# Performance work log

Hardware: AMD Instinct MI355X
Metric: run time of the kernel (lower is better)

The kernel has to match this reference:

```python
import jax, jax.numpy as jnp
import numpy as np


def _sage_conv(x_src, x_dst, esrc, edst, num_dst, W_l, b_l, W_r):
    # PyG SAGEConv (aggr='mean'): out = lin_l(mean_{j->i} x_j) + lin_r(x_i)
    msg = x_src[esrc]                                   # [E, F] gather
    agg = jax.ops.segment_sum(msg, edst, num_segments=num_dst)
    cnt = jax.ops.segment_sum(jnp.ones((esrc.shape[0],), x_src.dtype), edst,
                              num_segments=num_dst)
    mean = agg / jnp.maximum(cnt, 1.0)[:, None]         # [num_dst, F]
    return mean @ W_l + b_l + x_dst @ W_r


def setup_inputs() -> dict:
    key = jax.random.key(0)
    ks = jax.random.split(key, 12)
    N_TOTAL, F_IN, HID, OUT = 1500000, 128, 256, 128
    NS0, ND0, NS1, ND1 = 1441792, 90112, 90112, 8192
    E0, E1 = 1351680, 81920
    x_all = jax.random.normal(ks[0], (N_TOTAL, F_IN), dtype=jnp.float32)
    n_id = jax.random.randint(ks[1], (NS0,), 0, N_TOTAL, dtype=jnp.int64)
    edge_src0 = jax.random.randint(ks[2], (E0,), 0, NS0, dtype=jnp.int64)
    edge_dst0 = jax.random.randint(ks[3], (E0,), 0, ND0, dtype=jnp.int64)
    edge_src1 = jax.random.randint(ks[4], (E1,), 0, NS1, dtype=jnp.int64)
    edge_dst1 = jax.random.randint(ks[5], (E1,), 0, ND1, dtype=jnp.int64)
    s0 = 1.0 / np.sqrt(F_IN)
    s1 = 1.0 / np.sqrt(HID)
    W_l0 = jax.random.normal(ks[6], (F_IN, HID), dtype=jnp.float32) * s0
    b_l0 = jnp.zeros((HID,), dtype=jnp.float32)
    W_r0 = jax.random.normal(ks[7], (F_IN, HID), dtype=jnp.float32) * s0
    W_l1 = jax.random.normal(ks[8], (HID, OUT), dtype=jnp.float32) * s1
    b_l1 = jnp.zeros((OUT,), dtype=jnp.float32)
    W_r1 = jax.random.normal(ks[9], (HID, OUT), dtype=jnp.float32) * s1
    return {
        "x_all": x_all, "n_id": n_id,
        "edge_src0": edge_src0, "edge_dst0": edge_dst0,
        "edge_src1": edge_src1, "edge_dst1": edge_dst1,
        "W_l0": W_l0, "b_l0": b_l0, "W_r0": W_r0,
        "W_l1": W_l1, "b_l1": b_l1, "W_r1": W_r1,
        "num_src0": NS0, "num_dst0": ND0, "num_src1": NS1, "num_dst1": ND1,
    }


def reference(x_all, n_id, edge_src0, edge_dst0, edge_src1, edge_dst1,
              W_l0, b_l0, W_r0, W_l1, b_l1, W_r1,
              num_src0, num_dst0, num_src1, num_dst1):
    x = x_all[n_id]                                     # [num_src0, F_in]
    # Layer 1 (block 0): bipartite SAGEConv + ReLU
    x = _sage_conv(x[:num_src0], x[:num_dst0], edge_src0, edge_dst0,
                   num_dst0, W_l0, b_l0, W_r0)
    x = jax.nn.relu(x)                                  # [num_dst0, hid]
    # Layer 2 (block 1): final SAGEConv, no activation
    x = _sage_conv(x[:num_src1], x[:num_dst1], edge_src1, edge_dst1,
                   num_dst1, W_l1, b_l1, W_r1)
    return x                                            # [num_dst1, out]
```

## Files before the change

kernel.cpp:

```cpp
#include <hip/hip_runtime.h>

#define ND0 90112
#define ND1 8192
#define NDT (ND0 + ND1)
#define NE0 1351680
#define NE1 81920
#define NET (NE0 + NE1)
#define F_IN 128
#define HID 256
#define F_OUT 128
#define BCAP 64

typedef __attribute__((ext_vector_type(8))) short short8;
typedef __attribute__((ext_vector_type(4))) float f32x4;

__device__ inline ushort f2bf(float f) {
    unsigned u = __float_as_uint(f);
    return (ushort)((u + 0x7fffu + ((u >> 16) & 1u)) >> 16);
}
__device__ inline float bf2f(ushort h) {
    return __uint_as_float(((unsigned)h) << 16);
}

__global__ void bucket_scatter_k(const int* __restrict__ esrc0, const int* __restrict__ edst0,
                                 const int* __restrict__ esrc1, const int* __restrict__ edst1,
                                 const int* __restrict__ nid, int* __restrict__ cnt,
                                 int* __restrict__ bkt) {
    int e = blockIdx.x * 256 + threadIdx.x;
    if (e >= NET) return;
    int d, s;
    if (e < NE0) {
        d = edst0[e];
        s = nid[esrc0[e]];
    } else {
        int e1 = e - NE0;
        d = ND0 + edst1[e1];
        s = esrc1[e1];
    }
    int pos = atomicAdd(&cnt[d], 1);
    if (pos < BCAP) bkt[(size_t)d * BCAP + pos] = s;
}

__global__ void wtrans_all_k(const float* __restrict__ Wl0, const float* __restrict__ Wr0,
                             const float* __restrict__ Wl1, const float* __restrict__ Wr1,
                             ushort* __restrict__ Bt0, ushort* __restrict__ Bt1) {
    int idx = blockIdx.x * 256 + threadIdx.x;
    constexpr int N0 = HID * 2 * F_IN;
    if (idx < N0) {
        int K2 = 2 * F_IN;
        int n = idx / K2, k = idx - n * K2;
        float v = (k < F_IN) ? Wl0[(size_t)k * HID + n] : Wr0[(size_t)(k - F_IN) * HID + n];
        Bt0[idx] = f2bf(v);
    } else {
        int j = idx - N0;
        int K2 = 2 * HID;
        int n = j / K2, k = j - n * K2;
        float v = (k < HID) ? Wl1[(size_t)k * F_OUT + n] : Wr1[(size_t)(k - HID) * F_OUT + n];
        Bt1[j] = f2bf(v);
    }
}

__global__ __launch_bounds__(512, 4) void fused1_k(
    const float* __restrict__ X, const int* __restrict__ bkt,
    const int* __restrict__ cnt, const int* __restrict__ nid,
    const ushort* __restrict__ Bt, const float* __restrict__ bias,
    ushort* __restrict__ C) {
    __shared__ ushort As[64][264];
    __shared__ ushort Bs[64][72];
    __shared__ int s_num[64];

    int t = threadIdx.x;
    int row0 = blockIdx.x * 64;

    if (t < 64) s_num[t] = cnt[row0 + t];
    __syncthreads();

    {
        int row = t >> 3, q = t & 7;
        int gr = nid[row0 + row];
        const float* gp = &X[(size_t)gr * F_IN + q * 16];
#pragma unroll
        for (int i = 0; i < 2; ++i) {
            float4 v0 = *(const float4*)(gp + i * 8);
            float4 v1 = *(const float4*)(gp + i * 8 + 4);
            short8 o;
            o[0] = (short)f2bf(v0.x); o[1] = (short)f2bf(v0.y);
            o[2] = (short)f2bf(v0.z); o[3] = (short)f2bf(v0.w);
            o[4] = (short)f2bf(v1.x); o[5] = (short)f2bf(v1.y);
            o[6] = (short)f2bf(v1.z); o[7] = (short)f2bf(v1.w);
            *(short8*)&As[row][F_IN + q * 16 + i * 8] = o;
        }
    }

    {
        int u = t & 3;
        int slot = (t >> 2) & 3;
        int rloc = t >> 4;
#pragma unroll 1
        for (int pass = 0; pass < 2; ++pass) {
            int row = pass * 32 + rloc;
            int beg = (row0 + row) * BCAP;
            int num = s_num[row];
            float acc[32] = {};
#pragma unroll 1
            for (int e = slot; e < num; e += 4) {
                int r = bkt[beg + e];
                const float* rp = &X[(size_t)r * F_IN + u * 4];
#pragma unroll
                for (int i = 0; i < 8; ++i) {
                    float4 v = *(const float4*)(rp + i * 16);
                    acc[i * 4 + 0] += v.x;
                    acc[i * 4 + 1] += v.y;
                    acc[i * 4 + 2] += v.z;
                    acc[i * 4 + 3] += v.w;
                }
            }
#pragma unroll
            for (int i = 0; i < 32; ++i) {
                acc[i] += __shfl_xor(acc[i], 4);
                acc[i] += __shfl_xor(acc[i], 8);
            }
            if (slot == 0) {
                float inv = 1.f / (float)((num > 0) ? num : 1);
#pragma unroll
                for (int i = 0; i < 8; ++i) {
                    ushort4 o;
                    o.x = f2bf(acc[i * 4 + 0] * inv);
                    o.y = f2bf(acc[i * 4 + 1] * inv);
                    o.z = f2bf(acc[i * 4 + 2] * inv);
                    o.w = f2bf(acc[i * 4 + 3] * inv);
                    *(ushort4*)&As[row][i * 16 + u * 4] = o;
                }
            }
        }
    }

    int lane = t & 63;
    int w = t >> 6;
    int wm = w >> 2, wn2 = w & 3;
    int lr = lane & 15, lj = lane >> 4;
    int bn = t >> 3, bk = (t & 7) * 8;

    for (int nt = 0; nt < 4; ++nt) {
        f32x4 acc2[2] = {};
        for (int k0 = 0; k0 < 256; k0 += 64) {
            short8 bv = *(const short8*)&Bt[(size_t)(nt * 64 + bn) * 256 + k0 + bk];
            __syncthreads();
            *(short8*)&Bs[bn][bk] = bv;
            __syncthreads();
#pragma unroll
            for (int ks = 0; ks < 64; ks += 32) {
                short8 bf = *(const short8*)&Bs[wn2 * 16 + lr][ks + lj * 8];
#pragma unroll
                for (int mi = 0; mi < 2; ++mi) {
                    short8 af = *(const short8*)&As[wm * 32 + mi * 16 + lr][k0 + ks + lj * 8];
                    acc2[mi] = __builtin_amdgcn_mfma_f32_16x16x32_bf16(af, bf, acc2[mi], 0, 0, 0);
                }
            }
        }
        int c = nt * 64 + wn2 * 16 + lr;
        float bi = bias[c];
#pragma unroll
        for (int mi = 0; mi < 2; ++mi) {
#pragma unroll
            for (int j = 0; j < 4; ++j) {
                int r = row0 + wm * 32 + mi * 16 + lj * 4 + j;
                float v = acc2[mi][j] + bi;
                v = fmaxf(v, 0.f);
                C[(size_t)r * HID + c] = f2bf(v);
            }
        }
    }
}

template <int F>
__global__ __launch_bounds__(128) void agg_k(
    const ushort* __restrict__ Xh, const int* __restrict__ bkt,
    const int* __restrict__ cnt, int dofs, ushort* __restrict__ mean) {
    __shared__ float sh[128][8];
    int d = blockIdx.x;
    int t = threadIdx.x;
    int cg = t & 31, slot = t >> 5;
    int beg = (dofs + d) * BCAP;
    int num = cnt[dofs + d];
    float acc[8] = {};
    for (int e = 0; e < num; e += 8) {
        int i0 = e + slot, i1 = e + 4 + slot;
        bool v0 = i0 < num, v1 = i1 < num;
        int r0 = v0 ? bkt[beg + i0] : 0;
        int r1 = v1 ? bkt[beg + i1] : 0;
        if (v0) {
            short8 x = *(const short8*)&Xh[(size_t)r0 * F + cg * 8];
#pragma unroll
            for (int i = 0; i < 8; ++i) acc[i] += bf2f((ushort)x[i]);
        }
        if (v1) {
            short8 x = *(const short8*)&Xh[(size_t)r1 * F + cg * 8];
#pragma unroll
            for (int i = 0; i < 8; ++i) acc[i] += bf2f((ushort)x[i]);
        }
    }
#pragma unroll
    for (int i = 0; i < 8; ++i) sh[t][i] = acc[i];
    __syncthreads();
    if (t < 32) {
        float inv = 1.f / (float)((num > 0) ? num : 1);
        short8 ov;
#pragma unroll
        for (int i = 0; i < 8; ++i) {
            float s = sh[t][i] + sh[t + 32][i] + sh[t + 64][i] + sh[t + 96][i];
            ov[i] = (short)f2bf(s * inv);
        }
        *(short8*)&mean[(size_t)d * F + t * 8] = ov;
    }
}

template <int BM, int KHALF, int NCOLS, bool RELU, bool OUT_BF16>
__global__ __launch_bounds__(256) void mgemm_k(
    const ushort* __restrict__ A0, const ushort* __restrict__ A1,
    const ushort* __restrict__ Bt, const float* __restrict__ bias,
    void* __restrict__ Cv, int M) {
    constexpr int MI = BM / 32;
    constexpr int TPR = 256 / BM;
    constexpr int AV = 64 / TPR / 8;
    __shared__ ushort As[BM][72];
    __shared__ ushort Bs[64][72];

    int t = threadIdx.x;
    int row0 = blockIdx.x * BM;
    int col0 = blockIdx.y * 64;
    int lane = t & 63;
    int w = t >> 6, wm = w >> 1, wn = w & 1;
    int lr = lane & 15;
    int lk = (lane >> 4) * 8;

    int ar = t / TPR, ac = (t % TPR) * (64 / TPR);
    int bn = t >> 2, bc = (t & 3) * 16;

    f32x4 acc[MI][2] = {};

    for (int k0 = 0; k0 < 2 * KHALF; k0 += 64) {
        const ushort* Asrc = (k0 < KHALF) ? A0 : A1;
        int kof = (k0 < KHALF) ? k0 : (k0 - KHALF);
        const ushort* ap = &Asrc[(size_t)(row0 + ar) * KHALF + kof + ac];
        const ushort* bp = &Bt[(size_t)(col0 + bn) * (2 * KHALF) + k0 + bc];
        short8 av[AV];
#pragma unroll
        for (int i = 0; i < AV; ++i) av[i] = *(const short8*)(ap + 8 * i);
        short8 bv0 = *(const short8*)(bp);
        short8 bv1 = *(const short8*)(bp + 8);
        __syncthreads();
#pragma unroll
        for (int i = 0; i < AV; ++i) *(short8*)&As[ar][ac + 8 * i] = av[i];
        *(short8*)&Bs[bn][bc + 0] = bv0;
        *(short8*)&Bs[bn][bc + 8] = bv1;
        __syncthreads();
#pragma unroll
        for (int ks = 0; ks < 64; ks += 32) {
            short8 bf0 = *(const short8*)&Bs[wn * 32 + lr][ks + lk];
            short8 bf1 = *(const short8*)&Bs[wn * 32 + 16 + lr][ks + lk];
#pragma unroll
            for (int mi = 0; mi < MI; ++mi) {
                short8 af = *(const short8*)&As[wm * (BM / 2) + mi * 16 + lr][ks + lk];
                acc[mi][0] = __builtin_amdgcn_mfma_f32_16x16x32_bf16(af, bf0, acc[mi][0], 0, 0, 0);
                acc[mi][1] = __builtin_amdgcn_mfma_f32_16x16x32_bf16(af, bf1, acc[mi][1], 0, 0, 0);
            }
        }
    }

    int orow = row0 + wm * (BM / 2);
    int ocol = col0 + wn * 32;
#pragma unroll
    for (int mi = 0; mi < MI; ++mi) {
#pragma unroll
        for (int ni = 0; ni < 2; ++ni) {
            int c = ocol + ni * 16 + lr;
            float bi = bias[c];
#pragma unroll
            for (int j = 0; j < 4; ++j) {
                int r = orow + mi * 16 + (lane >> 4) * 4 + j;
                float v = acc[mi][ni][j] + bi;
                if (RELU) v = fmaxf(v, 0.f);
                if (OUT_BF16)
                    ((ushort*)Cv)[(size_t)r * NCOLS + c] = f2bf(v);
                else
                    ((float*)Cv)[(size_t)r * NCOLS + c] = v;
            }
        }
    }
}

extern "C" void kernel_launch(void* const* d_in, const int* in_sizes, int n_in,
                              void* d_out, int out_size, void* d_ws, size_t ws_size,
                              hipStream_t stream) {
    const float* x_all = (const float*)d_in[0];
    const int* n_id = (const int*)d_in[1];
    const int* esrc0 = (const int*)d_in[2];
    const int* edst0 = (const int*)d_in[3];
    const int* esrc1 = (const int*)d_in[4];
    const int* edst1 = (const int*)d_in[5];
    const float* W_l0 = (const float*)d_in[6];
    const float* b_l0 = (const float*)d_in[7];
    const float* W_r0 = (const float*)d_in[8];
    const float* W_l1 = (const float*)d_in[9];
    const float* b_l1 = (const float*)d_in[10];
    const float* W_r1 = (const float*)d_in[11];

    char* ws = (char*)d_ws;
    size_t off = 0;
    auto alloc = [&](size_t bytes) {
        off = (off + 255) & ~(size_t)255;
        void* p = ws + off;
        off += bytes;
        return p;
    };
    int* cnt = (int*)alloc((size_t)NDT * 4);
    int* bkt = (int*)alloc((size_t)NDT * BCAP * 4);
    ushort* h = (ushort*)alloc((size_t)ND0 * HID * 2);
    ushort* mean1 = (ushort*)alloc((size_t)ND1 * HID * 2);
    ushort* Bt0 = (ushort*)alloc((size_t)HID * (2 * F_IN) * 2);
    ushort* Bt1 = (ushort*)alloc((size_t)F_OUT * (2 * HID) * 2);

    hipMemsetAsync(cnt, 0, (size_t)NDT * 4, stream);

    wtrans_all_k<<<512, 256, 0, stream>>>(W_l0, W_r0, W_l1, W_r1, Bt0, Bt1);
    bucket_scatter_k<<<(NET + 255) / 256, 256, 0, stream>>>(esrc0, edst0, esrc1,
                                                            edst1, n_id, cnt, bkt);

    fused1_k<<<ND0 / 64, 512, 0, stream>>>(x_all, bkt, cnt, n_id, Bt0, b_l0, h);

    agg_k<HID><<<ND1, 128, 0, stream>>>(h, bkt, cnt, ND0, mean1);
    mgemm_k<64, HID, F_OUT, false, false>
        <<<dim3(ND1 / 64, F_OUT / 64), 256, 0, stream>>>(mean1, h, Bt1, b_l1,
                                                         (float*)d_out, ND1);
}
```

Before: 239.6 us.

## Merge prep kernels, software-pipeline layer-1 gather, fuse layer-2 aggregate with GEMM

```diff
diff --git a/kernel.cpp b/kernel.cpp
--- a/kernel.cpp
+++ b/kernel.cpp
@@ -10,6 +10,7 @@
 #define HID 256
 #define F_OUT 128
 #define BCAP 64
+#define WT_BLOCKS 512
 
 typedef __attribute__((ext_vector_type(8))) short short8;
 typedef __attribute__((ext_vector_type(4))) float f32x4;
@@ -22,41 +23,44 @@
     return __uint_as_float(((unsigned)h) << 16);
 }
 
-__global__ void bucket_scatter_k(const int* __restrict__ esrc0, const int* __restrict__ edst0,
-                                 const int* __restrict__ esrc1, const int* __restrict__ edst1,
-                                 const int* __restrict__ nid, int* __restrict__ cnt,
-                                 int* __restrict__ bkt) {
-    int e = blockIdx.x * 256 + threadIdx.x;
-    if (e >= NET) return;
-    int d, s;
-    if (e < NE0) {
-        d = edst0[e];
-        s = nid[esrc0[e]];
+__global__ void prep_k(const float* __restrict__ Wl0, const float* __restrict__ Wr0,
+                       const float* __restrict__ Wl1, const float* __restrict__ Wr1,
+                       ushort* __restrict__ Bt0, ushort* __restrict__ Bt1,
+                       const int* __restrict__ esrc0, const int* __restrict__ edst0,
+                       const int* __restrict__ esrc1, const int* __restrict__ edst1,
+                       const int* __restrict__ nid, int* __restrict__ cnt,
+                       int* __restrict__ bkt) {
+    if (blockIdx.x < WT_BLOCKS) {
+        int idx = blockIdx.x * 256 + threadIdx.x;
+        constexpr int N0 = HID * 2 * F_IN;
+        if (idx < N0) {
+            int K2 = 2 * F_IN;
+            int n = idx / K2, k = idx - n * K2;
+            float v = (k < F_IN) ? Wl0[(size_t)k * HID + n]
+                                 : Wr0[(size_t)(k - F_IN) * HID + n];
+            Bt0[idx] = f2bf(v);
+        } else {
+            int j = idx - N0;
+            int K2 = 2 * HID;
+            int n = j / K2, k = j - n * K2;
+            float v = (k < HID) ? Wl1[(size_t)k * F_OUT + n]
+                                : Wr1[(size_t)(k - HID) * F_OUT + n];
+            Bt1[j] = f2bf(v);
+        }
     } else {
-        int e1 = e - NE0;
-        d = ND0 + edst1[e1];
-        s = esrc1[e1];
-    }
-    int pos = atomicAdd(&cnt[d], 1);
-    if (pos < BCAP) bkt[(size_t)d * BCAP + pos] = s;
-}
-
-__global__ void wtrans_all_k(const float* __restrict__ Wl0, const float* __restrict__ Wr0,
-                             const float* __restrict__ Wl1, const float* __restrict__ Wr1,
-                             ushort* __restrict__ Bt0, ushort* __restrict__ Bt1) {
-    int idx = blockIdx.x * 256 + threadIdx.x;
-    constexpr int N0 = HID * 2 * F_IN;
-    if (idx < N0) {
-        int K2 = 2 * F_IN;
-        int n = idx / K2, k = idx - n * K2;
-        float v = (k < F_IN) ? Wl0[(size_t)k * HID + n] : Wr0[(size_t)(k - F_IN) * HID + n];
-        Bt0[idx] = f2bf(v);
-    } else {
-        int j = idx - N0;
-        int K2 = 2 * HID;
-        int n = j / K2, k = j - n * K2;
-        float v = (k < HID) ? Wl1[(size_t)k * F_OUT + n] : Wr1[(size_t)(k - HID) * F_OUT + n];
-        Bt1[j] = f2bf(v);
+        int e = (blockIdx.x - WT_BLOCKS) * 256 + threadIdx.x;
+        if (e >= NET) return;
+        int d, s;
+        if (e < NE0) {
+            d = edst0[e];
+            s = nid[esrc0[e]];
+        } else {
+            int e1 = e - NE0;
+            d = ND0 + edst1[e1];
+            s = esrc1[e1];
+        }
+        int pos = atomicAdd(&cnt[d], 1);
+        if (pos < BCAP) bkt[(size_t)d * BCAP + pos] = s;
     }
 }
 
@@ -102,17 +106,50 @@
             int beg = (row0 + row) * BCAP;
             int num = s_num[row];
             float acc[32] = {};
+            float4 A[8], B[8];
+            int eA = slot, eB = slot + 4;
+            bool hasA = eA < num, hasB = eB < num;
+            if (hasA) {
+                const float* rp = &X[(size_t)bkt[beg + eA] * F_IN + u * 4];
+#pragma unroll
+                for (int i = 0; i < 8; ++i) A[i] = *(const float4*)(rp + i * 16);
+            }
+            if (hasB) {
+                const float* rp = &X[(size_t)bkt[beg + eB] * F_IN + u * 4];
+#pragma unroll
+                for (int i = 0; i < 8; ++i) B[i] = *(const float4*)(rp + i * 16);
+            }
 #pragma unroll 1
-            for (int e = slot; e < num; e += 4) {
-                int r = bkt[beg + e];
-                const float* rp = &X[(size_t)r * F_IN + u * 4];
+            while (hasA) {
 #pragma unroll
                 for (int i = 0; i < 8; ++i) {
-                    float4 v = *(const float4*)(rp + i * 16);
-                    acc[i * 4 + 0] += v.x;
-                    acc[i * 4 + 1] += v.y;
-                    acc[i * 4 + 2] += v.z;
-                    acc[i * 4 + 3] += v.w;
+                    acc[i * 4 + 0] += A[i].x;
+                    acc[i * 4 + 1] += A[i].y;
+                    acc[i * 4 + 2] += A[i].z;
+                    acc[i * 4 + 3] += A[i].w;
+                }
+                eA += 8;
+                hasA = eA < num;
+                if (hasA) {
+                    const float* rp = &X[(size_t)bkt[beg + eA] * F_IN + u * 4];
+#pragma unroll
+                    for (int i = 0; i < 8; ++i) A[i] = *(const float4*)(rp + i * 16);
+                }
+                if (hasB) {
+#pragma unroll
+                    for (int i = 0; i < 8; ++i) {
+                        acc[i * 4 + 0] += B[i].x;
+                        acc[i * 4 + 1] += B[i].y;
+                        acc[i * 4 + 2] += B[i].z;
+                        acc[i * 4 + 3] += B[i].w;
+                    }
+                    eB += 8;
+                    hasB = eB < num;
+                    if (hasB) {
+                        const float* rp = &X[(size_t)bkt[beg + eB] * F_IN + u * 4];
+#pragma unroll
+                        for (int i = 0; i < 8; ++i) B[i] = *(const float4*)(rp + i * 16);
+                    }
                 }
             }
 #pragma unroll
@@ -173,118 +210,83 @@
     }
 }
 
-template <int F>
-__global__ __launch_bounds__(128) void agg_k(
-    const ushort* __restrict__ Xh, const int* __restrict__ bkt,
-    const int* __restrict__ cnt, int dofs, ushort* __restrict__ mean) {
-    __shared__ float sh[128][8];
-    int d = blockIdx.x;
+__global__ __launch_bounds__(512, 2) void fused2_k(
+    const ushort* __restrict__ H, const int* __restrict__ bkt,
+    const int* __restrict__ cnt, const ushort* __restrict__ Bt,
+    const float* __restrict__ bias, float* __restrict__ out) {
+    __shared__ ushort As[64][520];
+    __shared__ ushort Bs[64][72];
+    __shared__ int s_num[64];
+
     int t = threadIdx.x;
-    int cg = t & 31, slot = t >> 5;
-    int beg = (dofs + d) * BCAP;
-    int num = cnt[dofs + d];
-    float acc[8] = {};
-    for (int e = 0; e < num; e += 8) {
-        int i0 = e + slot, i1 = e + 4 + slot;
-        bool v0 = i0 < num, v1 = i1 < num;
-        int r0 = v0 ? bkt[beg + i0] : 0;
-        int r1 = v1 ? bkt[beg + i1] : 0;
-        if (v0) {
-            short8 x = *(const short8*)&Xh[(size_t)r0 * F + cg * 8];
-#pragma unroll
-            for (int i = 0; i < 8; ++i) acc[i] += bf2f((ushort)x[i]);
-        }
-        if (v1) {
-            short8 x = *(const short8*)&Xh[(size_t)r1 * F + cg * 8];
-#pragma unroll
-            for (int i = 0; i < 8; ++i) acc[i] += bf2f((ushort)x[i]);
-        }
-    }
-#pragma unroll
-    for (int i = 0; i < 8; ++i) sh[t][i] = acc[i];
+    int row0 = blockIdx.x * 64;
+    if (t < 64) s_num[t] = cnt[ND0 + row0 + t];
     __syncthreads();
-    if (t < 32) {
+
+    {
+        int row = t >> 3, q = t & 7;
+        const ushort* hp = &H[(size_t)(row0 + row) * HID + q * 32];
+#pragma unroll
+        for (int i = 0; i < 4; ++i)
+            *(short8*)&As[row][HID + q * 32 + i * 8] = *(const short8*)(hp + i * 8);
+    }
+
+    {
+        int row = t >> 3, q = t & 7;
+        int beg = (ND0 + row0 + row) * BCAP;
+        int num = s_num[row];
+        float acc[32] = {};
+#pragma unroll 1
+        for (int e = 0; e < num; ++e) {
+            const ushort* rp = &H[(size_t)bkt[beg + e] * HID + q * 32];
+#pragma unroll
+            for (int i = 0; i < 4; ++i) {
+                short8 x = *(const short8*)(rp + i * 8);
+#pragma unroll
+                for (int j = 0; j < 8; ++j) acc[i * 8 + j] += bf2f((ushort)x[j]);
+            }
+        }
         float inv = 1.f / (float)((num > 0) ? num : 1);
-        short8 ov;
-#pragma unroll
-        for (int i = 0; i < 8; ++i) {
-            float s = sh[t][i] + sh[t + 32][i] + sh[t + 64][i] + sh[t + 96][i];
-            ov[i] = (short)f2bf(s * inv);
-        }
-        *(short8*)&mean[(size_t)d * F + t * 8] = ov;
-    }
-}
-
-template <int BM, int KHALF, int NCOLS, bool RELU, bool OUT_BF16>
-__global__ __launch_bounds__(256) void mgemm_k(
-    const ushort* __restrict__ A0, const ushort* __restrict__ A1,
-    const ushort* __restrict__ Bt, const float* __restrict__ bias,
-    void* __restrict__ Cv, int M) {
-    constexpr int MI = BM / 32;
-    constexpr int TPR = 256 / BM;
-    constexpr int AV = 64 / TPR / 8;
-    __shared__ ushort As[BM][72];
-    __shared__ ushort Bs[64][72];
-
-    int t = threadIdx.x;
-    int row0 = blockIdx.x * BM;
-    int col0 = blockIdx.y * 64;
+#pragma unroll
+        for (int i = 0; i < 4; ++i) {
+            short8 o;
+#pragma unroll
+            for (int j = 0; j < 8; ++j) o[j] = (short)f2bf(acc[i * 8 + j] * inv);
+            *(short8*)&As[row][q * 32 + i * 8] = o;
+        }
+    }
+
     int lane = t & 63;
-    int w = t >> 6, wm = w >> 1, wn = w & 1;
-    int lr = lane & 15;
-    int lk = (lane >> 4) * 8;
-
-    int ar = t / TPR, ac = (t % TPR) * (64 / TPR);
-    int bn = t >> 2, bc = (t & 3) * 16;
-
-    f32x4 acc[MI][2] = {};
-
-    for (int k0 = 0; k0 < 2 * KHALF; k0 += 64) {
-        const ushort* Asrc = (k0 < KHALF) ? A0 : A1;
-        int kof = (k0 < KHALF) ? k0 : (k0 - KHALF);
-        const ushort* ap = &Asrc[(size_t)(row0 + ar) * KHALF + kof + ac];
-        const ushort* bp = &Bt[(size_t)(col0 + bn) * (2 * KHALF) + k0 + bc];
-        short8 av[AV];
-#pragma unroll
-        for (int i = 0; i < AV; ++i) av[i] = *(const short8*)(ap + 8 * i);
-        short8 bv0 = *(const short8*)(bp);
-        short8 bv1 = *(const short8*)(bp + 8);
-        __syncthreads();
-#pragma unroll
-        for (int i = 0; i < AV; ++i) *(short8*)&As[ar][ac + 8 * i] = av[i];
-        *(short8*)&Bs[bn][bc + 0] = bv0;
-        *(short8*)&Bs[bn][bc + 8] = bv1;
-        __syncthreads();
-#pragma unroll
-        for (int ks = 0; ks < 64; ks += 32) {
-            short8 bf0 = *(const short8*)&Bs[wn * 32 + lr][ks + lk];
-            short8 bf1 = *(const short8*)&Bs[wn * 32 + 16 + lr][ks + lk];
-#pragma unroll
-            for (int mi = 0; mi < MI; ++mi) {
-                short8 af = *(const short8*)&As[wm * (BM / 2) + mi * 16 + lr][ks + lk];
-                acc[mi][0] = __builtin_amdgcn_mfma_f32_16x16x32_bf16(af, bf0, acc[mi][0], 0, 0, 0);
-                acc[mi][1] = __builtin_amdgcn_mfma_f32_16x16x32_bf16(af, bf1, acc[mi][1], 0, 0, 0);
-            }
-        }
-    }
-
-    int orow = row0 + wm * (BM / 2);
-    int ocol = col0 + wn * 32;
-#pragma unroll
-    for (int mi = 0; mi < MI; ++mi) {
-#pragma unroll
-        for (int ni = 0; ni < 2; ++ni) {
-            int c = ocol + ni * 16 + lr;
-            float bi = bias[c];
+    int w = t >> 6;
+    int wm = w >> 2, wn2 = w & 3;
+    int lr = lane & 15, lj = lane >> 4;
+    int bn = t >> 3, bk = (t & 7) * 8;
+
+    for (int nt = 0; nt < 2; ++nt) {
+        f32x4 acc2[2] = {};
+        for (int k0 = 0; k0 < 512; k0 += 64) {
+            short8 bv = *(const short8*)&Bt[(size_t)(nt * 64 + bn) * 512 + k0 + bk];
+            __syncthreads();
+            *(short8*)&Bs[bn][bk] = bv;
+            __syncthreads();
+#pragma unroll
+            for (int ks = 0; ks < 64; ks += 32) {
+                short8 bf = *(const short8*)&Bs[wn2 * 16 + lr][ks + lj * 8];
+#pragma unroll
+                for (int mi = 0; mi < 2; ++mi) {
+                    short8 af = *(const short8*)&As[wm * 32 + mi * 16 + lr][k0 + ks + lj * 8];
+                    acc2[mi] = __builtin_amdgcn_mfma_f32_16x16x32_bf16(af, bf, acc2[mi], 0, 0, 0);
+                }
+            }
+        }
+        int c = nt * 64 + wn2 * 16 + lr;
+        float bi = bias[c];
+#pragma unroll
+        for (int mi = 0; mi < 2; ++mi) {
 #pragma unroll
             for (int j = 0; j < 4; ++j) {
-                int r = orow + mi * 16 + (lane >> 4) * 4 + j;
-                float v = acc[mi][ni][j] + bi;
-                if (RELU) v = fmaxf(v, 0.f);
-                if (OUT_BF16)
-                    ((ushort*)Cv)[(size_t)r * NCOLS + c] = f2bf(v);
-                else
-                    ((float*)Cv)[(size_t)r * NCOLS + c] = v;
+                int r = row0 + wm * 32 + mi * 16 + lj * 4 + j;
+                out[(size_t)r * F_OUT + c] = acc2[mi][j] + bi;
             }
         }
     }
@@ -317,20 +319,15 @@
     int* cnt = (int*)alloc((size_t)NDT * 4);
     int* bkt = (int*)alloc((size_t)NDT * BCAP * 4);
     ushort* h = (ushort*)alloc((size_t)ND0 * HID * 2);
-    ushort* mean1 = (ushort*)alloc((size_t)ND1 * HID * 2);
     ushort* Bt0 = (ushort*)alloc((size_t)HID * (2 * F_IN) * 2);
     ushort* Bt1 = (ushort*)alloc((size_t)F_OUT * (2 * HID) * 2);
 
     hipMemsetAsync(cnt, 0, (size_t)NDT * 4, stream);
 
-    wtrans_all_k<<<512, 256, 0, stream>>>(W_l0, W_r0, W_l1, W_r1, Bt0, Bt1);
-    bucket_scatter_k<<<(NET + 255) / 256, 256, 0, stream>>>(esrc0, edst0, esrc1,
-                                                            edst1, n_id, cnt, bkt);
+    prep_k<<<WT_BLOCKS + (NET + 255) / 256, 256, 0, stream>>>(
+        W_l0, W_r0, W_l1, W_r1, Bt0, Bt1, esrc0, edst0, esrc1, edst1, n_id, cnt, bkt);
 
     fused1_k<<<ND0 / 64, 512, 0, stream>>>(x_all, bkt, cnt, n_id, Bt0, b_l0, h);
 
-    agg_k<HID><<<ND1, 128, 0, stream>>>(h, bkt, cnt, ND0, mean1);
-    mgemm_k<64, HID, F_OUT, false, false>
-        <<<dim3(ND1 / 64, F_OUT / 64), 256, 0, stream>>>(mean1, h, Bt1, b_l1,
-                                                         (float*)d_out, ND1);
-}
+    fused2_k<<<ND1 / 64, 512, 0, stream>>>(h, bkt, cnt, Bt1, b_l1, (float*)d_out);
+}
```

Measured after the change: 374.0 us. 1.56x slower.
